# Performance work log

Hardware: AMD Instinct MI355X
Metric: run time of the kernel (lower is better)

The kernel has to match this reference:

```python
import jax, jax.numpy as jnp
import numpy as np


def _shift(x, n):
    # torch.roll along the last (angular) axis
    return jnp.roll(x, n, axis=3)


def _flip(x, n):
    # mirror about index n along the last axis: out[..., i] = x[..., (n - i) mod W]
    return jnp.roll(jnp.flip(x, axis=3), n + 1, axis=3)


def setup_inputs() -> dict:
    key = jax.random.key(0)
    k1, k2, k3 = jax.random.split(key, 3)
    B, C, H, W = 16, 96, 96, 96
    x = jax.random.normal(k1, (B, C, H, W), dtype=jnp.float32)
    s = jax.random.normal(k2, (B, 5), dtype=jnp.float32)
    w = jax.random.uniform(k3, (B, C, H, W), dtype=jnp.float32) + 0.1  # keep denominator well-conditioned
    return {"x": x, "s": s, "w": w}


def reference(x, s, w):
    # s.shape[1] == 5 branch of SymmetryControl (square symmetry: 3 rotations + 2 mirrors)
    sg = jax.nn.sigmoid(s).reshape(s.shape[0], -1, 1, 1)  # [B,5,1,1]
    step = x.shape[3] // 8

    x90 = _shift(x, step * 2)
    x180 = _shift(x, step * 4)
    x270 = _shift(x, step * 6)
    x90f = _flip(x, step * 2 - 1)
    x180f = _flip(x, step * 4 - 1)

    w90 = sg[:, 0:1] * _shift(w, step * 2)
    w180 = sg[:, 1:2] * _shift(w, step * 4)
    w270 = sg[:, 2:3] * _shift(w, step * 6)
    w90f = sg[:, 3:4] * _flip(w, step * 2 - 1)
    w180f = sg[:, 4:5] * _flip(w, step * 4 - 1)

    a = (w * x + w90 * x90 + w180 * x180 + w270 * x270
         + w90f * x90f + w180f * x180f)
    b = w + w90 + w180 + w270 + w90f + w180f
    return a / b
```

## Files before the change

kernel.cpp:

```cpp
#include <hip/hip_runtime.h>


#define WDIM 96
#define QDIM 24
#define ROWS 8
#define RPB  9216

__global__ __launch_bounds__(QDIM * ROWS, 6)
void symctl_kernel(const float* __restrict__ x,
                   const float* __restrict__ s,
                   const float* __restrict__ w,
                   float* __restrict__ out) {
    const int qx      = threadIdx.x;
    const int rowbase = blockIdx.x * ROWS;
    const int row     = rowbase + threadIdx.y;
    const int b       = rowbase / RPB;

    const float* sb = s + b * 5;
    const float sg0 = 1.0f / (1.0f + __expf(-sb[0]));
    const float sg1 = 1.0f / (1.0f + __expf(-sb[1]));
    const float sg2 = 1.0f / (1.0f + __expf(-sb[2]));
    const float sg3 = 1.0f / (1.0f + __expf(-sb[3]));
    const float sg4 = 1.0f / (1.0f + __expf(-sb[4]));

    int qa = qx - 6;  if (qa < 0) qa += QDIM;
    int qb = qx - 12; if (qb < 0) qb += QDIM;
    int qc = qx + 6;  if (qc >= QDIM) qc -= QDIM;
    int qd = 5  - qx; if (qd < 0) qd += QDIM;
    int qe = 11 - qx; if (qe < 0) qe += QDIM;

    const float4* __restrict__ xr = (const float4*)(x + (size_t)row * WDIM);
    const float4* __restrict__ wr = (const float4*)(w + (size_t)row * WDIM);

    const float4 X0 = xr[qx], Xa = xr[qa], Xb = xr[qb], Xc = xr[qc], Xd = xr[qd], Xe = xr[qe];
    const float4 W0 = wr[qx], Wa = wr[qa], Wb = wr[qb], Wc = wr[qc], Wd = wr[qd], We = wr[qe];

    const float* x0p = (const float*)&X0; const float* w0p = (const float*)&W0;
    const float* xap = (const float*)&Xa; const float* wap = (const float*)&Wa;
    const float* xbp = (const float*)&Xb; const float* wbp = (const float*)&Wb;
    const float* xcp = (const float*)&Xc; const float* wcp = (const float*)&Wc;
    const float* xdp = (const float*)&Xd; const float* wdp = (const float*)&Wd;
    const float* xep = (const float*)&Xe; const float* wep = (const float*)&We;

    float4 res;
    float* rp = (float*)&res;
#pragma unroll
    for (int j = 0; j < 4; ++j) {
        const int r = 3 - j;
        const float w0 = w0p[j];
        const float ga = sg0 * wap[j], gb = sg1 * wbp[j], gc = sg2 * wcp[j];
        const float gd = sg3 * wdp[r], ge = sg4 * wep[r];

        float num = w0 * x0p[j];
        num = fmaf(ga, xap[j], num);
        num = fmaf(gb, xbp[j], num);
        num = fmaf(gc, xcp[j], num);
        num = fmaf(gd, xdp[r], num);
        num = fmaf(ge, xep[r], num);

        const float den = w0 + ga + gb + gc + gd + ge;
        rp[j] = num * __builtin_amdgcn_rcpf(den);
    }

    float4* outr = (float4*)(out + (size_t)row * WDIM);
    outr[qx] = res;
}

extern "C" void kernel_launch(void* const* d_in, const int* in_sizes, int n_in,
                              void* d_out, int out_size, void* d_ws, size_t ws_size,
                              hipStream_t stream) {
    const float* x = (const float*)d_in[0];
    const float* s = (const float*)d_in[1];
    const float* w = (const float*)d_in[2];
    float* out = (float*)d_out;

    const int n_rows = in_sizes[0] / WDIM;
    const int grid = n_rows / ROWS;

    dim3 block(QDIM, ROWS);
    symctl_kernel<<<grid, block, 0, stream>>>(x, s, w, out);
}
```

Measured before the change: 157.5 us.

## Stage x*w products in shared memory and compute symmetric orbits per thread

Each thread now loads one float4 of x and w, stores the product x*w and w into LDS, and after a barrier every thread gathers the 4-rotation orbit and its mirror from shared memory, so each output needs only sigmoid-weighted FMAs. This replaces six global float4 gathers per operand with a single coalesced load, cutting redundant global/L2 traffic. Output is now written as scalar strided stores, 24 apart, instead of float4. Rows per block go from 8 to 16, and a __syncthreads plus LDS usage may reduce occupancy.

```diff
diff --git a/kernel.cpp b/kernel.cpp
--- a/kernel.cpp
+++ b/kernel.cpp
@@ -2,18 +2,22 @@
 
 
 #define WDIM 96
-#define QDIM 24
-#define ROWS 8
+#define ROWS 16
 #define RPB  9216
+#define LSTR 100
 
-__global__ __launch_bounds__(QDIM * ROWS, 6)
+__global__ __launch_bounds__(24 * ROWS)
 void symctl_kernel(const float* __restrict__ x,
                    const float* __restrict__ s,
                    const float* __restrict__ w,
                    float* __restrict__ out) {
-    const int qx      = threadIdx.x;
+    __shared__ float pb[ROWS][LSTR];
+    __shared__ float wb[ROWS][LSTR];
+
+    const int t       = threadIdx.x;
+    const int ry      = threadIdx.y;
     const int rowbase = blockIdx.x * ROWS;
-    const int row     = rowbase + threadIdx.y;
+    const int row     = rowbase + ry;
     const int b       = rowbase / RPB;
 
     const float* sb = s + b * 5;
@@ -23,47 +27,55 @@
     const float sg3 = 1.0f / (1.0f + __expf(-sb[3]));
     const float sg4 = 1.0f / (1.0f + __expf(-sb[4]));
 
-    int qa = qx - 6;  if (qa < 0) qa += QDIM;
-    int qb = qx - 12; if (qb < 0) qb += QDIM;
-    int qc = qx + 6;  if (qc >= QDIM) qc -= QDIM;
-    int qd = 5  - qx; if (qd < 0) qd += QDIM;
-    int qe = 11 - qx; if (qe < 0) qe += QDIM;
+    const float4 x4 = ((const float4*)(x + (size_t)row * WDIM))[t];
+    const float4 w4 = ((const float4*)(w + (size_t)row * WDIM))[t];
+    float4 p4;
+    p4.x = x4.x * w4.x; p4.y = x4.y * w4.y;
+    p4.z = x4.z * w4.z; p4.w = x4.w * w4.w;
+    *(float4*)&pb[ry][4 * t] = p4;
+    *(float4*)&wb[ry][4 * t] = w4;
 
-    const float4* __restrict__ xr = (const float4*)(x + (size_t)row * WDIM);
-    const float4* __restrict__ wr = (const float4*)(w + (size_t)row * WDIM);
+    __syncthreads();
 
-    const float4 X0 = xr[qx], Xa = xr[qa], Xb = xr[qb], Xc = xr[qc], Xd = xr[qd], Xe = xr[qe];
-    const float4 W0 = wr[qx], Wa = wr[qa], Wb = wr[qb], Wc = wr[qc], Wd = wr[qd], We = wr[qe];
+    const int r  = t;
+    const int rm = 23 - t;
+    const float* pr = &pb[ry][0];
+    const float* wr = &wb[ry][0];
 
-    const float* x0p = (const float*)&X0; const float* w0p = (const float*)&W0;
-    const float* xap = (const float*)&Xa; const float* wap = (const float*)&Wa;
-    const float* xbp = (const float*)&Xb; const float* wbp = (const float*)&Wb;
-    const float* xcp = (const float*)&Xc; const float* wcp = (const float*)&Wc;
-    const float* xdp = (const float*)&Xd; const float* wdp = (const float*)&Wd;
-    const float* xep = (const float*)&Xe; const float* wep = (const float*)&We;
-
-    float4 res;
-    float* rp = (float*)&res;
+    float pq[4], aq[4], pP[4], aP[4];
 #pragma unroll
-    for (int j = 0; j < 4; ++j) {
-        const int r = 3 - j;
-        const float w0 = w0p[j];
-        const float ga = sg0 * wap[j], gb = sg1 * wbp[j], gc = sg2 * wcp[j];
-        const float gd = sg3 * wdp[r], ge = sg4 * wep[r];
-
-        float num = w0 * x0p[j];
-        num = fmaf(ga, xap[j], num);
-        num = fmaf(gb, xbp[j], num);
-        num = fmaf(gc, xcp[j], num);
-        num = fmaf(gd, xdp[r], num);
-        num = fmaf(ge, xep[r], num);
-
-        const float den = w0 + ga + gb + gc + gd + ge;
-        rp[j] = num * __builtin_amdgcn_rcpf(den);
+    for (int q = 0; q < 4; ++q) {
+        pq[q] = pr[24 * q + r];
+        aq[q] = wr[24 * q + r];
+        pP[q] = pr[24 * q + rm];
+        aP[q] = wr[24 * q + rm];
     }
 
-    float4* outr = (float4*)(out + (size_t)row * WDIM);
-    outr[qx] = res;
+    float* orow = out + (size_t)row * WDIM + r;
+#pragma unroll
+    for (int q = 0; q < 4; ++q) {
+        const int i1 = (q + 3) & 3;
+        const int i2 = (q + 2) & 3;
+        const int i3 = (q + 1) & 3;
+        const int i4 = (4 - q) & 3;
+        const int i5 = (5 - q) & 3;
+
+        float num = pq[q];
+        num = fmaf(sg0, pq[i1], num);
+        num = fmaf(sg1, pq[i2], num);
+        num = fmaf(sg2, pq[i3], num);
+        num = fmaf(sg3, pP[i4], num);
+        num = fmaf(sg4, pP[i5], num);
+
+        float den = aq[q];
+        den = fmaf(sg0, aq[i1], den);
+        den = fmaf(sg1, aq[i2], den);
+        den = fmaf(sg2, aq[i3], den);
+        den = fmaf(sg3, aP[i4], den);
+        den = fmaf(sg4, aP[i5], den);
+
+        orow[24 * q] = num * __builtin_amdgcn_rcpf(den);
+    }
 }
 
 extern "C" void kernel_launch(void* const* d_in, const int* in_sizes, int n_in,
@@ -77,6 +89,6 @@
     const int n_rows = in_sizes[0] / WDIM;
     const int grid = n_rows / ROWS;
 
-    dim3 block(QDIM, ROWS);
+    dim3 block(24, ROWS);
     symctl_kernel<<<grid, block, 0, stream>>>(x, s, w, out);
 }
```

After: 149.0 us. -5.4%, faster.
